# Performance work log

Measured on AMD Instinct MI355X. Metric: run time of the kernel, lower is better.

The kernel has to match this reference:

```python
import jax, jax.numpy as jnp
import numpy as np

N = 65536
DEG = 16
E = N * DEG
C_IN = 128
C_OUT = 64
HEADS = 1


def setup_inputs() -> dict:
    key = jax.random.key(0)
    k1, k2, k3, k4 = jax.random.split(key, 4)
    rng = np.random.default_rng(0)
    row = rng.integers(0, N, E)
    off = rng.integers(1, N, E)
    col = (row + off) % N  # guarantees no self-loops
    order = np.lexsort((col, row))  # pre-sorted like gnn.sort_edge_index
    edge_index = np.stack([row[order], col[order]], axis=1).astype(np.int64)  # [E,2]
    x = jax.random.normal(k1, (N, C_IN), jnp.float32)
    edge_dist = jax.random.uniform(k2, (E,), jnp.float32, minval=0.5, maxval=2.0)
    w_bound = float(np.sqrt(6.0 / (C_IN + C_OUT)))  # xavier_uniform
    a_bound = float(np.sqrt(6.0 / (2 * C_OUT + 1)))
    weight = jax.random.uniform(k3, (HEADS, C_IN, C_OUT), jnp.float32, -w_bound, w_bound)
    attention = jax.random.uniform(k4, (HEADS, 2 * C_OUT, 1), jnp.float32, -a_bound, a_bound)
    return {
        "x": x,
        "edge_index": jnp.asarray(edge_index),
        "edge_dist": edge_dist,
        "weight": weight,
        "attention": attention,
    }


def reference(x, edge_index, edge_dist, weight, attention):
    n = x.shape[0]
    heads, _, h = weight.shape  # heads == 1 (module only valid for heads=1)
    row = edge_index[:, 0]
    col = edge_index[:, 1]
    # sort_edge_index: stable lexicographic sort by (row, col)
    perm = jnp.argsort(row * n + col)
    row, col, ed = row[perm], col[perm], edge_dist[perm]
    # add_self_loops (inputs contain no self loops); self-loop edge_dist fill = 1.0
    loop = jnp.arange(n, dtype=row.dtype)
    row = jnp.concatenate([row, loop])
    col = jnp.concatenate([col, loop])
    ed = jnp.concatenate([ed, jnp.ones((n,), ed.dtype)])  # [E']
    # out = x @ weight -> [heads, N, h]
    out = jnp.einsum('nc,kco->kno', x, weight)
    oe = out[:, row]                         # gather: [heads, E', h]
    oe = jnp.concatenate([oe, oe], axis=-1)  # duplicate -> [heads, E', 2h]
    oe = oe.reshape(-1, 2 * h)               # [E', 2h] (heads=1)
    alpha = (oe @ attention[0]).reshape(-1)  # [E']
    # segment softmax over destination node `row`
    m = jax.ops.segment_max(alpha, row, num_segments=n)
    e = jnp.exp(alpha - m[row])
    z = jax.ops.segment_sum(e, row, num_segments=n)
    alpha = e / (z[row] + 1e-16)
    oe = oe * alpha[:, None]
    s = oe.reshape(-1, heads, 2 * h).sum(axis=-1) / ed[:, None]  # [E', heads]
    d = s[row] - s[col]  # indexes edge array by node ids (faithful to source)
    return d.reshape(-1, h)
```

## Files before the change

### kernel.cpp

```cpp
#include <hip/hip_runtime.h>

#define C_IN 128
#define C_OUT 64
#define SPLIT 32768

__device__ __forceinline__ int probe_stride(const int* __restrict__ ei) {
    return ((ei[1] == 0) & (ei[3] == 0) & (ei[5] == 0) & (ei[7] == 0)) ? 4 : 2;
}

__global__ void k_bound(const int* __restrict__ ei, const float* __restrict__ W,
                        float* __restrict__ w_sum, int* __restrict__ start,
                        int* __restrict__ end, int* __restrict__ pS, int E) {
    int tid = threadIdx.x;
    if (blockIdx.x == 0 && tid < C_IN) {
        float s = 0.f;
        #pragma unroll
        for (int o = 0; o < C_OUT; ++o) s += W[tid * C_OUT + o];
        w_sum[tid] = s;
    }
    int e = blockIdx.x * blockDim.x + tid;
    if (e >= E) return;
    int st = probe_stride(ei);
    int r = ei[st * e];
    if (e == 0) {
        start[r] = 0;
        if (r >= SPLIT) pS[0] = 0;
    } else {
        int rp = ei[st * (e - 1)];
        if (r != rp) {
            end[rp] = e;
            start[r] = e;
            if (r >= SPLIT && rp < SPLIT) pS[0] = e;
        }
    }
    if (e == E - 1) {
        end[r] = E;
        if (r < SPLIT) pS[0] = E;
    }
}

__global__ void k_t(const float* __restrict__ x, const float* __restrict__ w_sum,
                    const int* __restrict__ start, const int* __restrict__ end,
                    float* __restrict__ t, int N) {
    __shared__ float ws[C_IN];
    if (threadIdx.x < C_IN) ws[threadIdx.x] = w_sum[threadIdx.x];
    __syncthreads();
    int gid = blockIdx.x * blockDim.x + threadIdx.x;
    int node = gid >> 2;
    int sub  = gid & 3;
    if (node < N) {
        const float4* xr = (const float4*)(x + (size_t)node * C_IN);
        float s = 0.f;
        #pragma unroll
        for (int j = 0; j < 8; ++j) {
            float4 v = xr[sub + 4 * j];
            const float* wp = ws + (sub + 4 * j) * 4;
            s += v.x * wp[0] + v.y * wp[1] + v.z * wp[2] + v.w * wp[3];
        }
        s += __shfl_xor(s, 1);
        s += __shfl_xor(s, 2);
        if (sub == 0) {
            float z = (float)(end[node] - start[node] + 1) + 1e-16f;
            t[node] = 2.0f * s / z;
        }
    }
}

__global__ void k_lookup(const int* __restrict__ ei, const int* __restrict__ pS,
                         const float* __restrict__ ed, const float* __restrict__ t,
                         float* __restrict__ lk, int N, int E) {
    int j = blockIdx.x * blockDim.x + threadIdx.x;
    if (j >= N) return;
    int S = pS[0], st = probe_stride(ei);
    int orig = S + j; if (orig >= E) orig -= E;
    lk[j] = t[ei[st * orig]] / ed[orig];
}

__global__ void k_out(const int* __restrict__ ei, const int* __restrict__ pS,
                      const float* __restrict__ lk, float* __restrict__ out,
                      int E, int N) {
    int k = blockIdx.x * blockDim.x + threadIdx.x;
    if (k < E) {
        int S = pS[0], st = probe_stride(ei);
        int orig = k + S; if (orig >= E) orig -= E;
        int r = ei[st * orig];
        int c = ei[st * orig + (st >> 1)];
        out[k] = lk[r] - lk[c];
    } else if (k < E + N) {
        out[k] = 0.0f;
    }
}

extern "C" void kernel_launch(void* const* d_in, const int* in_sizes, int n_in,
                              void* d_out, int out_size, void* d_ws, size_t ws_size,
                              hipStream_t stream) {
    const float* x  = (const float*)d_in[0];
    const int*   ei = (const int*)d_in[1];
    const float* ed = (const float*)d_in[2];
    const float* W  = (const float*)d_in[3];
    float* out = (float*)d_out;

    int N = in_sizes[0] / C_IN;
    int E = in_sizes[2];

    char* ws = (char*)d_ws;
    int*   start = (int*)ws;
    int*   end   = start + N;
    float* t     = (float*)(ws + (size_t)N * 8);
    float* lk    = (float*)(ws + (size_t)N * 12);
    float* w_sum = (float*)(ws + (size_t)N * 16);
    int*   pS    = (int*)(ws + (size_t)N * 16 + 512);

    k_bound<<<(E + 255) / 256, 256, 0, stream>>>(ei, W, w_sum, start, end, pS, E);
    k_t<<<(N * 4 + 255) / 256, 256, 0, stream>>>(x, w_sum, start, end, t, N);
    k_lookup<<<(N + 255) / 256, 256, 0, stream>>>(ei, pS, ed, t, lk, N, E);
    k_out<<<(E + N + 255) / 256, 256, 0, stream>>>(ei, pS, lk, out, E, N);
}
```

Before: 98.91 us.

## Fuse lookup-table build into node kernel and vectorize edge index loads

Removes the separate k_lookup kernel. Each node's threads now walk that node's edge range and write the lk entries whose shifted index falls below N, which avoids a kernel launch and the indirect gather t[ei[...]]. k_out now reads each (row, col) pair with a single int2 or int4 load instead of two strided scalar loads. The cost is a per-node loop over its edges, which adds some divergence, plus bounds checks that guard against start/end entries never written for nodes with no edges.

```diff
diff --git a/kernel.cpp b/kernel.cpp
--- a/kernel.cpp
+++ b/kernel.cpp
@@ -41,39 +41,34 @@
 
 __global__ void k_t(const float* __restrict__ x, const float* __restrict__ w_sum,
                     const int* __restrict__ start, const int* __restrict__ end,
-                    float* __restrict__ t, int N) {
+                    const float* __restrict__ ed, const int* __restrict__ pS,
+                    float* __restrict__ t, float* __restrict__ lk, int N, int E) {
     __shared__ float ws[C_IN];
     if (threadIdx.x < C_IN) ws[threadIdx.x] = w_sum[threadIdx.x];
     __syncthreads();
     int gid = blockIdx.x * blockDim.x + threadIdx.x;
     int node = gid >> 2;
     int sub  = gid & 3;
-    if (node < N) {
-        const float4* xr = (const float4*)(x + (size_t)node * C_IN);
-        float s = 0.f;
-        #pragma unroll
-        for (int j = 0; j < 8; ++j) {
-            float4 v = xr[sub + 4 * j];
-            const float* wp = ws + (sub + 4 * j) * 4;
-            s += v.x * wp[0] + v.y * wp[1] + v.z * wp[2] + v.w * wp[3];
-        }
-        s += __shfl_xor(s, 1);
-        s += __shfl_xor(s, 2);
-        if (sub == 0) {
-            float z = (float)(end[node] - start[node] + 1) + 1e-16f;
-            t[node] = 2.0f * s / z;
-        }
+    if (node >= N) return;
+    const float4* xr = (const float4*)(x + (size_t)node * C_IN);
+    float s = 0.f;
+    #pragma unroll
+    for (int j = 0; j < 8; ++j) {
+        float4 v = xr[sub + 4 * j];
+        const float* wp = ws + (sub + 4 * j) * 4;
+        s += v.x * wp[0] + v.y * wp[1] + v.z * wp[2] + v.w * wp[3];
     }
-}
-
-__global__ void k_lookup(const int* __restrict__ ei, const int* __restrict__ pS,
-                         const float* __restrict__ ed, const float* __restrict__ t,
-                         float* __restrict__ lk, int N, int E) {
-    int j = blockIdx.x * blockDim.x + threadIdx.x;
-    if (j >= N) return;
-    int S = pS[0], st = probe_stride(ei);
-    int orig = S + j; if (orig >= E) orig -= E;
-    lk[j] = t[ei[st * orig]] / ed[orig];
+    s += __shfl_xor(s, 1);
+    s += __shfl_xor(s, 2);
+    int b = start[node], en = end[node];
+    if (b < 0 || en > E || b >= en) return;
+    float tv = 2.0f * s / ((float)(en - b + 1) + 1e-16f);
+    if (sub == 0) t[node] = tv;
+    int S = pS[0];
+    for (int e = b + sub; e < en; e += 4) {
+        int j = e - S; if (j < 0) j += E;
+        if (j < N) lk[j] = tv / ed[e];
+    }
 }
 
 __global__ void k_out(const int* __restrict__ ei, const int* __restrict__ pS,
@@ -81,10 +76,16 @@
                       int E, int N) {
     int k = blockIdx.x * blockDim.x + threadIdx.x;
     if (k < E) {
-        int S = pS[0], st = probe_stride(ei);
+        int S = pS[0];
         int orig = k + S; if (orig >= E) orig -= E;
-        int r = ei[st * orig];
-        int c = ei[st * orig + (st >> 1)];
+        int r, c;
+        if (probe_stride(ei) == 2) {
+            int2 rc = ((const int2*)ei)[orig];
+            r = rc.x; c = rc.y;
+        } else {
+            int4 rc = ((const int4*)ei)[orig];
+            r = rc.x; c = rc.z;
+        }
         out[k] = lk[r] - lk[c];
     } else if (k < E + N) {
         out[k] = 0.0f;
@@ -112,7 +113,6 @@
     int*   pS    = (int*)(ws + (size_t)N * 16 + 512);
 
     k_bound<<<(E + 255) / 256, 256, 0, stream>>>(ei, W, w_sum, start, end, pS, E);
-    k_t<<<(N * 4 + 255) / 256, 256, 0, stream>>>(x, w_sum, start, end, t, N);
-    k_lookup<<<(N + 255) / 256, 256, 0, stream>>>(ei, pS, ed, t, lk, N, E);
+    k_t<<<(N * 4 + 255) / 256, 256, 0, stream>>>(x, w_sum, start, end, ed, pS, t, lk, N, E);
     k_out<<<(E + N + 255) / 256, 256, 0, stream>>>(ei, pS, lk, out, E, N);
 }
```

Result: faster. 95.88 us (-3.1%).
